# Kernel tuning notes

Hardware: AMD Instinct MI355X
Metric: run time of the kernel (lower is better)

Reference implementation:

```python
import jax, jax.numpy as jnp
import numpy as np

D = 768
H = 16
DH = D // H  # 48


def setup_inputs() -> dict:
    key = jax.random.key(0)
    ks = jax.random.split(key, 7)
    s = 0.02
    x = jax.random.normal(ks[0], (4, 2048, D), dtype=jnp.float32)
    # weights stored as (in, out); torch Linear is y = x @ W.T + b
    W_qkv = jax.random.normal(ks[1], (D, 3 * D), dtype=jnp.float32) * s
    b_qkv = jax.random.normal(ks[2], (3 * D,), dtype=jnp.float32) * s
    W_o = jax.random.normal(ks[3], (D, D), dtype=jnp.float32) * s
    b_o = jax.random.normal(ks[4], (D,), dtype=jnp.float32) * s
    W_p = jax.random.normal(ks[5], (D, D), dtype=jnp.float32) * s
    b_p = jax.random.normal(ks[6], (D,), dtype=jnp.float32) * s
    return {"x": x, "W_qkv": W_qkv, "b_qkv": b_qkv, "W_o": W_o, "b_o": b_o, "W_p": W_p, "b_p": b_p}


def reference(x, W_qkv, b_qkv, W_o, b_o, W_p, b_p):
    b, n, _ = x.shape
    qkv = x @ W_qkv + b_qkv                     # (b, n, 3*D)
    # reshape to (b, n, H, 3*DH) as in torch, then chunk last dim into q,k,v
    # -> per-head interleaved layout [q_h | k_h | v_h]
    qkv = qkv.reshape(b, n, H, 3, DH).transpose(0, 2, 1, 3, 4)  # (b, H, n, 3, DH)
    q, k, v = qkv[..., 0, :], qkv[..., 1, :], qkv[..., 2, :]    # (b, H, n, DH)
    alpha = jnp.einsum("bhqd,bhkd->bhqk", q, k) / jnp.sqrt(jnp.float32(DH))
    alpha = jax.nn.softmax(alpha, axis=-1)      # dropout: eval mode (identity)
    out = jnp.einsum("bhqk,bhkd->bhqd", alpha, v)
    out = out.transpose(0, 2, 1, 3).reshape(b, n, D)
    out = out @ W_o + b_o
    out = out @ W_p + b_p
    return out
```

## Files before the change

### kernel.cpp

```cpp
#include <hip/hip_runtime.h>

#define DEV __device__ __forceinline__

typedef __attribute__((ext_vector_type(4))) float f32x4;
typedef __attribute__((ext_vector_type(8))) short bf16x8;
typedef __attribute__((ext_vector_type(4))) short bf16x4;
typedef __attribute__((ext_vector_type(4))) unsigned int u32x4;

DEV short f2bf(float f) {
  union { float f; unsigned u; } c; c.f = f;
  unsigned r = c.u + 0x7FFFu + ((c.u >> 16) & 1u);
  return (short)(r >> 16);
}

DEV unsigned cvtpk(float lo, float hi) {
  unsigned r;
  asm("v_cvt_pk_bf16_f32 %0, %1, %2" : "=v"(r) : "v"(lo), "v"(hi));
  return r;
}

DEV float exp2r(float x) { return __builtin_amdgcn_exp2f(x); }

DEV void gl_lds16(short* lds, const short* g) {
  __builtin_amdgcn_global_load_lds(
      (__attribute__((address_space(1))) void*)(void*)g,
      (__attribute__((address_space(3))) void*)lds, 16, 0, 0);
}

__global__ __launch_bounds__(256) void k_cvt(const float* __restrict__ in, short* __restrict__ out) {
  int i = blockIdx.x * 256 + threadIdx.x;
  float4 v = reinterpret_cast<const float4*>(in)[i];
  bf16x4 o;
  o[0] = f2bf(v.x); o[1] = f2bf(v.y); o[2] = f2bf(v.z); o[3] = f2bf(v.w);
  reinterpret_cast<bf16x4*>(out)[i] = o;
}

__global__ __launch_bounds__(256) void k_tcvt(const float* __restrict__ W, short* __restrict__ WT,
                                              int Kd, int Nd) {
  __shared__ float t[32][33];
  int nb = blockIdx.x * 32, kb = blockIdx.y * 32;
  int tx = threadIdx.x, ty = threadIdx.y;
#pragma unroll
  for (int i = ty; i < 32; i += 8) t[i][tx] = W[(long)(kb + i) * Nd + nb + tx];
  __syncthreads();
#pragma unroll
  for (int i = ty; i < 32; i += 8) WT[(long)(nb + i) * Kd + kb + tx] = f2bf(t[tx][i]);
}

__global__ __launch_bounds__(256) void k_bias(const float* __restrict__ bo, const float* __restrict__ bp,
                                              const float* __restrict__ Wp, float* __restrict__ bc) {
  int j = blockIdx.x * 256 + threadIdx.x;
  int k0 = blockIdx.y * 48;
  float s = 0.f;
#pragma unroll
  for (int k = 0; k < 48; ++k) s += bo[k0 + k] * Wp[(long)(k0 + k) * 768 + j];
  if (blockIdx.y == 0) s += bp[j];
  atomicAdd(&bc[j], s);
}

template <int MODE>
__global__ __launch_bounds__(256) void k_gemm(
    const short* __restrict__ A, const short* __restrict__ BT, const float* __restrict__ bias,
    short* __restrict__ Cb, float* __restrict__ Cf,
    short* __restrict__ Qp, short* __restrict__ Kp, short* __restrict__ VT,
    int M, int N, int K) {
  __shared__ short As[128 * 32];
  __shared__ short Bs[128 * 32];
  const int tid = threadIdx.x;
  const int w = tid >> 6, lane = tid & 63;
  const int lr = lane & 15, g = lane >> 4;
  const int m0 = blockIdx.y * 128, n0 = blockIdx.x * 128;
  const int wm = (w >> 1) * 64, wn = (w & 1) * 64;

  f32x4 acc[4][4];
#pragma unroll
  for (int i = 0; i < 4; ++i)
#pragma unroll
    for (int j = 0; j < 4; ++j)
#pragma unroll
      for (int r = 0; r < 4; ++r) acc[i][j][r] = 0.f;

  const short* Ab = A + (long)m0 * K;
  const short* Bb = BT + (long)n0 * K;
  const int row_s = tid >> 2;
  const int c_s = tid & 3;
  const int nk = K >> 5;

  for (int kt = 0; kt < nk; ++kt) {
    const int k0 = kt << 5;
#pragma unroll
    for (int i = 0; i < 2; ++i) {
      int row = row_s + i * 64;
      int cs = c_s ^ ((row >> 1) & 3);
      gl_lds16(As + (i * 256 + w * 64) * 8, Ab + (long)row * K + k0 + cs * 8);
      gl_lds16(Bs + (i * 256 + w * 64) * 8, Bb + (long)row * K + k0 + cs * 8);
    }
    __syncthreads();
    bf16x8 af[4], bf[4];
#pragma unroll
    for (int mi = 0; mi < 4; ++mi) {
      int r = wm + mi * 16 + lr;
      int c = g ^ ((r >> 1) & 3);
      af[mi] = *reinterpret_cast<const bf16x8*>(As + r * 32 + c * 8);
    }
#pragma unroll
    for (int nj = 0; nj < 4; ++nj) {
      int r = wn + nj * 16 + lr;
      int c = g ^ ((r >> 1) & 3);
      bf[nj] = *reinterpret_cast<const bf16x8*>(Bs + r * 32 + c * 8);
    }
#pragma unroll
    for (int mi = 0; mi < 4; ++mi)
#pragma unroll
      for (int nj = 0; nj < 4; ++nj)
        acc[mi][nj] = __builtin_amdgcn_mfma_f32_16x16x32_bf16(af[mi], bf[nj], acc[mi][nj], 0, 0, 0);
    __syncthreads();
  }

#pragma unroll
  for (int nj = 0; nj < 4; ++nj) {
    int col = n0 + wn + nj * 16 + lr;
    float bv = (MODE == 3) ? 0.f : bias[col];
    if (MODE == 0) {
      int h = col / 144;
      int rem = col - h * 144;
      int s = rem / 48;
      int d = rem - s * 48;
#pragma unroll
      for (int mi = 0; mi < 4; ++mi)
#pragma unroll
        for (int r = 0; r < 4; ++r) {
          int row = m0 + wm + mi * 16 + g * 4 + r;
          float val = acc[mi][nj][r] + bv;
          int b = row >> 11, n = row & 2047;
          int bh = (b << 4) + h;
          if (s == 0) {
            long o = ((long)(bh * 2048 + n)) * 64 + d;
            Qp[o] = f2bf(val * 0.20823051649867783f);
            if (d < 16) Qp[o + 48] = 0;
          } else if (s == 1) {
            long o = ((long)(bh * 2048 + n)) * 64 + d;
            Kp[o] = f2bf(val);
            if (d < 16) Kp[o + 48] = 0;
          } else {
            VT[((long)(bh * 48 + d)) * 2048 + n] = f2bf(val);
          }
        }
    } else {
#pragma unroll
      for (int mi = 0; mi < 4; ++mi)
#pragma unroll
        for (int r = 0; r < 4; ++r) {
          int row = m0 + wm + mi * 16 + g * 4 + r;
          float val = acc[mi][nj][r] + bv;
          if (MODE == 2) Cf[(long)row * N + col] = val;
          else           Cb[(long)row * N + col] = f2bf(val);
        }
    }
  }
}

__global__ __launch_bounds__(512, 8) void k_attn(const short* __restrict__ Q, const short* __restrict__ K,
                                                 const short* __restrict__ VT, short* __restrict__ AO) {
  const int tid = threadIdx.x, w = tid >> 6, lane = tid & 63;
  const int lr = lane & 15, g = lane >> 4;
  const int orig = blockIdx.x;
  const int logical = (orig & 7) * 128 + (orig >> 3);
  const int bh = logical >> 4;
  const int q0 = (logical & 15) * 128 + w * 16;

  const short* Qh = Q + (long)bh * 2048 * 64;
  const short* Kh = K + (long)bh * 2048 * 64;
  const short* VTh = VT + (long)bh * 48 * 2048;

  __shared__ short Ks[2][64 * 64];
  __shared__ short Vs[2][48 * 64];

  const int r_l = lane >> 3, c_l = lane & 7;
  const int gc8 = (c_l ^ r_l) * 8;

  bf16x8 bq0 = *reinterpret_cast<const bf16x8*>(Qh + (q0 + lr) * 64 + g * 8);
  bf16x8 bq1 = *reinterpret_cast<const bf16x8*>(Qh + (q0 + lr) * 64 + 32 + g * 8);

  bf16x8 vones;
#pragma unroll
  for (int i = 0; i < 8; ++i) vones[i] = (short)0x3F80;

  f32x4 acc[3];
#pragma unroll
  for (int df = 0; df < 3; ++df)
#pragma unroll
    for (int r = 0; r < 4; ++r) acc[df][r] = 0.f;
  f32x4 accl = {0.f, 0.f, 0.f, 0.f};

  const int srow = w * 8 + r_l;
  const short* kg = Kh + (long)srow * 64 + gc8;
  const short* vg = VTh + (long)srow * 2048 + gc8;

  gl_lds16(&Ks[0][w * 512], kg);
  if (w < 6) gl_lds16(&Vs[0][w * 512], vg);
  kg += 4096; vg += 64;
  asm volatile("s_waitcnt vmcnt(0)" ::: "memory");
  __syncthreads();

  const int sw = lr & 7;
  const int goff = (g & 1) * 4;
  const int ghalf = g >> 1;

  for (int t = 0; t < 32; ++t) {
    const int cur = t & 1;
    if (t < 31) {
      gl_lds16(&Ks[cur ^ 1][w * 512], kg);
      if (w < 6) gl_lds16(&Vs[cur ^ 1][w * 512], vg);
      kg += 4096; vg += 64;
    }

    const short* KsC = Ks[cur];
    const short* VsC = Vs[cur];

    f32x4 st[4];
    __builtin_amdgcn_s_setprio(1);
#pragma unroll
    for (int kf = 0; kf < 4; ++kf) {
      f32x4 sc = {0.f, 0.f, 0.f, 0.f};
      const short* kr = KsC + (kf * 16 + lr) * 64;
      bf16x8 a0 = *reinterpret_cast<const bf16x8*>(kr + (g ^ sw) * 8);
      bf16x8 a1 = *reinterpret_cast<const bf16x8*>(kr + ((4 + g) ^ sw) * 8);
      sc = __builtin_amdgcn_mfma_f32_16x16x32_bf16(a0, bq0, sc, 0, 0, 0);
      sc = __builtin_amdgcn_mfma_f32_16x16x32_bf16(a1, bq1, sc, 0, 0, 0);
      st[kf] = sc;
    }
    __builtin_amdgcn_s_setprio(0);

#pragma unroll
    for (int kf = 0; kf < 4; ++kf)
#pragma unroll
      for (int r = 0; r < 4; ++r) st[kf][r] = exp2r(st[kf][r]);

    __builtin_amdgcn_s_setprio(1);
#pragma unroll
    for (int ks = 0; ks < 2; ++ks) {
      u32x4 bw;
      bw[0] = cvtpk(st[2 * ks][0], st[2 * ks][1]);
      bw[1] = cvtpk(st[2 * ks][2], st[2 * ks][3]);
      bw[2] = cvtpk(st[2 * ks + 1][0], st[2 * ks + 1][1]);
      bw[3] = cvtpk(st[2 * ks + 1][2], st[2 * ks + 1][3]);
      bf16x8 bp = __builtin_bit_cast(bf16x8, bw);
      const int off_lo = ((ks * 4 + ghalf) ^ sw) * 8 + goff;
      const int off_hi = ((ks * 4 + 2 + ghalf) ^ sw) * 8 + goff;
      accl = __builtin_amdgcn_mfma_f32_16x16x32_bf16(vones, bp, accl, 0, 0, 0);
#pragma unroll
      for (int df = 0; df < 3; ++df) {
        const short* vbase = VsC + (df * 16 + lr) * 64;
        union { bf16x8 v; bf16x4 h[2]; } av;
        av.h[0] = *reinterpret_cast<const bf16x4*>(vbase + off_lo);
        av.h[1] = *reinterpret_cast<const bf16x4*>(vbase + off_hi);
        acc[df] = __builtin_amdgcn_mfma_f32_16x16x32_bf16(av.v, bp, acc[df], 0, 0, 0);
      }
    }
    __builtin_amdgcn_s_setprio(0);

    asm volatile("s_waitcnt vmcnt(0)" ::: "memory");
    __syncthreads();
  }

  int b = bh >> 4, h = bh & 15;
  float inv = 1.f / accl[0];
  long rowoff = ((long)((b << 11) + q0 + lr)) * 768 + h * 48;
#pragma unroll
  for (int df = 0; df < 3; ++df) {
    bf16x4 o;
#pragma unroll
    for (int r = 0; r < 4; ++r) o[r] = f2bf(acc[df][r] * inv);
    *reinterpret_cast<bf16x4*>(AO + rowoff + df * 16 + g * 4) = o;
  }
}

extern "C" void kernel_launch(void* const* d_in, const int* in_sizes, int n_in,
                              void* d_out, int out_size, void* d_ws, size_t ws_size,
                              hipStream_t stream) {
  const float* x    = (const float*)d_in[0];
  const float* Wqkv = (const float*)d_in[1];
  const float* bqkv = (const float*)d_in[2];
  const float* Wo   = (const float*)d_in[3];
  const float* bo   = (const float*)d_in[4];
  const float* Wp   = (const float*)d_in[5];
  const float* bp   = (const float*)d_in[6];

  char* ws = (char*)d_ws;
  short* xb    = (short*)(ws + 0);
  short* WqkvT = (short*)(ws + 12582912);
  short* WoT   = (short*)(ws + 16121856);
  short* WpT   = (short*)(ws + 17301504);
  short* Qp    = (short*)(ws + 18481152);
  short* Kp    = (short*)(ws + 35258368);
  short* VT    = (short*)(ws + 52035584);
  short* AO    = (short*)(ws + 64618496);
  short* Wob   = (short*)(ws + 0);
  short* WoWpT = (short*)(ws + 2097152);
  float* bc    = (float*)(ws + 4194304);

  k_cvt<<<6144, 256, 0, stream>>>(x, xb);
  k_tcvt<<<dim3(72, 24), dim3(32, 8), 0, stream>>>(Wqkv, WqkvT, 768, 2304);
  k_tcvt<<<dim3(24, 24), dim3(32, 8), 0, stream>>>(Wp, WpT, 768, 768);

  k_gemm<0><<<dim3(18, 64), 256, 0, stream>>>(xb, WqkvT, bqkv, nullptr, nullptr,
                                              Qp, Kp, VT, 8192, 2304, 768);
  k_cvt<<<576, 256, 0, stream>>>(Wo, Wob);
  k_gemm<3><<<dim3(6, 6), 256, 0, stream>>>(WpT, Wob, nullptr, WoWpT, nullptr,
                                            nullptr, nullptr, nullptr, 768, 768, 768);
  hipMemsetAsync(bc, 0, 768 * sizeof(float), stream);
  k_bias<<<dim3(3, 16), 256, 0, stream>>>(bo, bp, Wp, bc);

  k_attn<<<1024, 512, 0, stream>>>(Qp, Kp, VT, AO);
  k_gemm<2><<<dim3(6, 64), 256, 0, stream>>>(AO, WoWpT, bc, nullptr, (float*)d_out,
                                             nullptr, nullptr, nullptr, 8192, 768, 768);
}
```

Baseline: 209.5 us.

## Process two query tiles per wave in attention to reuse K/V LDS fragments

```diff
diff --git a/kernel.cpp b/kernel.cpp
--- a/kernel.cpp
+++ b/kernel.cpp
@@ -160,14 +160,14 @@
   }
 }
 
-__global__ __launch_bounds__(512, 8) void k_attn(const short* __restrict__ Q, const short* __restrict__ K,
+__global__ __launch_bounds__(256, 4) void k_attn(const short* __restrict__ Q, const short* __restrict__ K,
                                                  const short* __restrict__ VT, short* __restrict__ AO) {
   const int tid = threadIdx.x, w = tid >> 6, lane = tid & 63;
   const int lr = lane & 15, g = lane >> 4;
   const int orig = blockIdx.x;
   const int logical = (orig & 7) * 128 + (orig >> 3);
   const int bh = logical >> 4;
-  const int q0 = (logical & 15) * 128 + w * 16;
+  const int q0 = (logical & 15) * 128 + w * 32;
 
   const short* Qh = Q + (long)bh * 2048 * 64;
   const short* Kh = K + (long)bh * 2048 * 64;
@@ -181,24 +181,31 @@
 
   bf16x8 bq0 = *reinterpret_cast<const bf16x8*>(Qh + (q0 + lr) * 64 + g * 8);
   bf16x8 bq1 = *reinterpret_cast<const bf16x8*>(Qh + (q0 + lr) * 64 + 32 + g * 8);
+  bf16x8 bq2 = *reinterpret_cast<const bf16x8*>(Qh + (q0 + 16 + lr) * 64 + g * 8);
+  bf16x8 bq3 = *reinterpret_cast<const bf16x8*>(Qh + (q0 + 16 + lr) * 64 + 32 + g * 8);
 
   bf16x8 vones;
 #pragma unroll
   for (int i = 0; i < 8; ++i) vones[i] = (short)0x3F80;
 
-  f32x4 acc[3];
+  f32x4 accA[3], accB[3];
 #pragma unroll
   for (int df = 0; df < 3; ++df)
 #pragma unroll
-    for (int r = 0; r < 4; ++r) acc[df][r] = 0.f;
-  f32x4 accl = {0.f, 0.f, 0.f, 0.f};
-
-  const int srow = w * 8 + r_l;
-  const short* kg = Kh + (long)srow * 64 + gc8;
-  const short* vg = VTh + (long)srow * 2048 + gc8;
-
-  gl_lds16(&Ks[0][w * 512], kg);
-  if (w < 6) gl_lds16(&Vs[0][w * 512], vg);
+    for (int r = 0; r < 4; ++r) { accA[df][r] = 0.f; accB[df][r] = 0.f; }
+  f32x4 acclA = {0.f, 0.f, 0.f, 0.f}, acclB = {0.f, 0.f, 0.f, 0.f};
+
+  const short* kg = Kh + (long)(w * 8 + r_l) * 64 + gc8;
+  const short* vg = VTh + (long)(w * 8 + r_l) * 2048 + gc8;
+
+  auto STAGE = [&](int b) {
+    gl_lds16(&Ks[b][w * 512], kg);
+    gl_lds16(&Ks[b][(w + 4) * 512], kg + 2048);
+    gl_lds16(&Vs[b][w * 512], vg);
+    if (w < 2) gl_lds16(&Vs[b][(w + 4) * 512], vg + 65536);
+  };
+
+  STAGE(0);
   kg += 4096; vg += 64;
   asm volatile("s_waitcnt vmcnt(0)" ::: "memory");
   __syncthreads();
@@ -210,52 +217,63 @@
   for (int t = 0; t < 32; ++t) {
     const int cur = t & 1;
     if (t < 31) {
-      gl_lds16(&Ks[cur ^ 1][w * 512], kg);
-      if (w < 6) gl_lds16(&Vs[cur ^ 1][w * 512], vg);
+      STAGE(cur ^ 1);
       kg += 4096; vg += 64;
     }
 
     const short* KsC = Ks[cur];
     const short* VsC = Vs[cur];
 
-    f32x4 st[4];
+    f32x4 stA[4], stB[4];
     __builtin_amdgcn_s_setprio(1);
 #pragma unroll
     for (int kf = 0; kf < 4; ++kf) {
-      f32x4 sc = {0.f, 0.f, 0.f, 0.f};
       const short* kr = KsC + (kf * 16 + lr) * 64;
       bf16x8 a0 = *reinterpret_cast<const bf16x8*>(kr + (g ^ sw) * 8);
       bf16x8 a1 = *reinterpret_cast<const bf16x8*>(kr + ((4 + g) ^ sw) * 8);
-      sc = __builtin_amdgcn_mfma_f32_16x16x32_bf16(a0, bq0, sc, 0, 0, 0);
-      sc = __builtin_amdgcn_mfma_f32_16x16x32_bf16(a1, bq1, sc, 0, 0, 0);
-      st[kf] = sc;
+      f32x4 sA = {0.f, 0.f, 0.f, 0.f}, sB = {0.f, 0.f, 0.f, 0.f};
+      sA = __builtin_amdgcn_mfma_f32_16x16x32_bf16(a0, bq0, sA, 0, 0, 0);
+      sB = __builtin_amdgcn_mfma_f32_16x16x32_bf16(a0, bq2, sB, 0, 0, 0);
+      sA = __builtin_amdgcn_mfma_f32_16x16x32_bf16(a1, bq1, sA, 0, 0, 0);
+      sB = __builtin_amdgcn_mfma_f32_16x16x32_bf16(a1, bq3, sB, 0, 0, 0);
+      stA[kf] = sA; stB[kf] = sB;
     }
     __builtin_amdgcn_s_setprio(0);
 
 #pragma unroll
     for (int kf = 0; kf < 4; ++kf)
 #pragma unroll
-      for (int r = 0; r < 4; ++r) st[kf][r] = exp2r(st[kf][r]);
+      for (int r = 0; r < 4; ++r) {
+        stA[kf][r] = exp2r(stA[kf][r]);
+        stB[kf][r] = exp2r(stB[kf][r]);
+      }
 
     __builtin_amdgcn_s_setprio(1);
 #pragma unroll
     for (int ks = 0; ks < 2; ++ks) {
-      u32x4 bw;
-      bw[0] = cvtpk(st[2 * ks][0], st[2 * ks][1]);
-      bw[1] = cvtpk(st[2 * ks][2], st[2 * ks][3]);
-      bw[2] = cvtpk(st[2 * ks + 1][0], st[2 * ks + 1][1]);
-      bw[3] = cvtpk(st[2 * ks + 1][2], st[2 * ks + 1][3]);
-      bf16x8 bp = __builtin_bit_cast(bf16x8, bw);
+      u32x4 bwA, bwB;
+      bwA[0] = cvtpk(stA[2 * ks][0], stA[2 * ks][1]);
+      bwA[1] = cvtpk(stA[2 * ks][2], stA[2 * ks][3]);
+      bwA[2] = cvtpk(stA[2 * ks + 1][0], stA[2 * ks + 1][1]);
+      bwA[3] = cvtpk(stA[2 * ks + 1][2], stA[2 * ks + 1][3]);
+      bwB[0] = cvtpk(stB[2 * ks][0], stB[2 * ks][1]);
+      bwB[1] = cvtpk(stB[2 * ks][2], stB[2 * ks][3]);
+      bwB[2] = cvtpk(stB[2 * ks + 1][0], stB[2 * ks + 1][1]);
+      bwB[3] = cvtpk(stB[2 * ks + 1][2], stB[2 * ks + 1][3]);
+      bf16x8 bpA = __builtin_bit_cast(bf16x8, bwA);
+      bf16x8 bpB = __builtin_bit_cast(bf16x8, bwB);
       const int off_lo = ((ks * 4 + ghalf) ^ sw) * 8 + goff;
       const int off_hi = ((ks * 4 + 2 + ghalf) ^ sw) * 8 + goff;
-      accl = __builtin_amdgcn_mfma_f32_16x16x32_bf16(vones, bp, accl, 0, 0, 0);
+      acclA = __builtin_amdgcn_mfma_f32_16x16x32_bf16(vones, bpA, acclA, 0, 0, 0);
+      acclB = __builtin_amdgcn_mfma_f32_16x16x32_bf16(vones, bpB, acclB, 0, 0, 0);
 #pragma unroll
       for (int df = 0; df < 3; ++df) {
         const short* vbase = VsC + (df * 16 + lr) * 64;
         union { bf16x8 v; bf16x4 h[2]; } av;
         av.h[0] = *reinterpret_cast<const bf16x4*>(vbase + off_lo);
         av.h[1] = *reinterpret_cast<const bf16x4*>(vbase + off_hi);
-        acc[df] = __builtin_amdgcn_mfma_f32_16x16x32_bf16(av.v, bp, acc[df], 0, 0, 0);
+        accA[df] = __builtin_amdgcn_mfma_f32_16x16x32_bf16(av.v, bpA, accA[df], 0, 0, 0);
+        accB[df] = __builtin_amdgcn_mfma_f32_16x16x32_bf16(av.v, bpB, accB[df], 0, 0, 0);
       }
     }
     __builtin_amdgcn_s_setprio(0);
@@ -265,14 +283,17 @@
   }
 
   int b = bh >> 4, h = bh & 15;
-  float inv = 1.f / accl[0];
-  long rowoff = ((long)((b << 11) + q0 + lr)) * 768 + h * 48;
+  float invA = 1.f / acclA[0];
+  float invB = 1.f / acclB[0];
+  long rowA = ((long)((b << 11) + q0 + lr)) * 768 + h * 48;
+  long rowB = ((long)((b << 11) + q0 + 16 + lr)) * 768 + h * 48;
 #pragma unroll
   for (int df = 0; df < 3; ++df) {
-    bf16x4 o;
-#pragma unroll
-    for (int r = 0; r < 4; ++r) o[r] = f2bf(acc[df][r] * inv);
-    *reinterpret_cast<bf16x4*>(AO + rowoff + df * 16 + g * 4) = o;
+    bf16x4 oA, oB;
+#pragma unroll
+    for (int r = 0; r < 4; ++r) { oA[r] = f2bf(accA[df][r] * invA); oB[r] = f2bf(accB[df][r] * invB); }
+    *reinterpret_cast<bf16x4*>(AO + rowA + df * 16 + g * 4) = oA;
+    *reinterpret_cast<bf16x4*>(AO + rowB + df * 16 + g * 4) = oB;
   }
 }
 
@@ -290,7 +311,6 @@
   char* ws = (char*)d_ws;
   short* xb    = (short*)(ws + 0);
   short* WqkvT = (short*)(ws + 12582912);
-  short* WoT   = (short*)(ws + 16121856);
   short* WpT   = (short*)(ws + 17301504);
   short* Qp    = (short*)(ws + 18481152);
   short* Kp    = (short*)(ws + 35258368);
@@ -312,7 +332,7 @@
   hipMemsetAsync(bc, 0, 768 * sizeof(float), stream);
   k_bias<<<dim3(3, 16), 256, 0, stream>>>(bo, bp, Wp, bc);
 
-  k_attn<<<1024, 512, 0, stream>>>(Qp, Kp, VT, AO);
+  k_attn<<<1024, 256, 0, stream>>>(Qp, Kp, VT, AO);
   k_gemm<2><<<dim3(6, 64), 256, 0, stream>>>(AO, WoWpT, bc, nullptr, (float*)d_out,
                                              nullptr, nullptr, nullptr, 8192, 768, 768);
 }
```

Result: faster. 193.0 us (-7.9%).
